# Performance work log

Hardware: AMD Instinct MI355X
Metric: run time of the kernel (lower is better)

Reference implementation:

```python
import jax, jax.numpy as jnp
import numpy as np

B, C_IN, C_OUT, K, H, W, STRIDE, PAD = 64, 64, 128, 3, 32, 32, 1, 1
H_OUT = (H + 2 * PAD - K) // STRIDE + 1
W_OUT = (W + 2 * PAD - K) // STRIDE + 1


def setup_inputs() -> dict:
    key = jax.random.key(0)
    k1, k2 = jax.random.split(key)
    x = jax.random.normal(k1, (B, C_IN, H, W), dtype=jnp.float32)
    fan_in = C_IN * K * K
    weight = jax.random.normal(k2, (C_OUT, H_OUT, W_OUT, C_IN, K, K), dtype=jnp.float32) / np.sqrt(fan_in).astype(np.float32)
    bias = jnp.zeros((C_OUT, H_OUT, W_OUT), dtype=jnp.float32)
    return {"x": x, "weight": weight, "bias": bias}


def _extract_patches(x):
    # x: [B, C, H, W] -> patches [B, C, H_OUT, W_OUT, K, K]
    xp = jnp.pad(x, ((0, 0), (0, 0), (PAD, PAD), (PAD, PAD)))
    rows = []
    for k in range(K):  # small fixed kernel loop (K=3), not a data-dim loop
        cols = []
        for l in range(K):
            cols.append(xp[:, :, k:k + H_OUT * STRIDE:STRIDE, l:l + W_OUT * STRIDE:STRIDE])
        rows.append(jnp.stack(cols, axis=-1))
    return jnp.stack(rows, axis=-2)


def reference(x, weight, bias):
    patches = _extract_patches(x)  # [B, C_IN, H_OUT, W_OUT, K, K]
    # per-location unshared GEMM: out[b,o,h,w] = sum_{i,k,l} weight[o,h,w,i,k,l] * patches[b,i,h,w,k,l]
    out = jnp.einsum('ohwikl,bihwkl->bohw', weight, patches)
    return out + bias[None]
```

## Files before the change

### kernel.cpp

```cpp
#include <hip/hip_runtime.h>


typedef __bf16  bf16x8  __attribute__((ext_vector_type(8)));
typedef float   floatx4 __attribute__((ext_vector_type(4)));

static __device__ inline bf16x8 cvt8(floatx4 a, floatx4 b) {
    bf16x8 r;
    r[0] = (__bf16)a[0]; r[1] = (__bf16)a[1]; r[2] = (__bf16)a[2]; r[3] = (__bf16)a[3];
    r[4] = (__bf16)b[0]; r[5] = (__bf16)b[1]; r[6] = (__bf16)b[2]; r[7] = (__bf16)b[3];
    return r;
}

__global__ __launch_bounds__(256, 3) void prep_kernel(
    const float* __restrict__ x, __bf16* __restrict__ P)
{
    __shared__ float xl[16 * 772];

    const int tid = threadIdx.x;
    const int bid = blockIdx.x;
    const int bq = bid & 3;
    const int ig = (bid >> 2) & 7;
    const int h  = bid >> 5;

    #pragma unroll
    for (int it = 0; it < 12; ++it) {
        int g   = tid + (it << 8);
        int row = g >> 3;
        int sub = g & 7;
        int bl  = row / 24;
        int rem = row - bl * 24;
        int il  = rem / 3;
        int ky  = rem - il * 3;
        int y   = h + ky - 1;
        floatx4 v = {0.f, 0.f, 0.f, 0.f};
        if ((unsigned)y < 32u) {
            const float* src = x + (((size_t)(bq * 16 + bl) * 64 + ig * 8 + il) << 10)
                                 + y * 32 + (sub << 2);
            v = *(const floatx4*)src;
        }
        *(floatx4*)&xl[bl * 772 + il * 96 + ky * 32 + (sub << 2)] = v;
    }
    __syncthreads();

    const int lane = tid & 63;
    const int wv = tid >> 6;
    const int bl = lane & 15;
    const int qq = lane >> 4;

    #pragma unroll 2
    for (int it = 0; it < 18; ++it) {
        int pr  = (it << 4) + (wv << 2) + qq;
        int w   = pr / 9;
        int kol = pr - w * 9;
        int ko  = ig * 9 + kol;
        bf16x8 piece;
        #pragma unroll
        for (int j = 0; j < 8; ++j) {
            int klocal = (kol << 3) + j;
            int il = klocal / 9;
            int p  = klocal - il * 9;
            int ky = p / 3;
            int kx = p - ky * 3;
            int xc = w + kx - 1;
            float v = ((unsigned)xc < 32u) ? xl[bl * 772 + il * 96 + ky * 32 + xc] : 0.0f;
            piece[j] = (__bf16)v;
        }
        int loc   = (h << 5) + w;
        int idx16 = ((ko >> 2) << 8) + (bq << 6) + ((ko & 3) << 4) + bl;
        *(bf16x8*)&P[((size_t)loc * 4608 + idx16) * 8] = piece;
    }
}

__global__ __launch_bounds__(256, 3) void local2d_kernel(
    const __bf16* __restrict__ P,
    const float* __restrict__ weight,
    const float* __restrict__ bias,
    float* __restrict__ out)
{
    __shared__ __bf16 alds[2][12288];

    const int tid  = threadIdx.x;
    const int lane = tid & 63;
    const int wv   = tid >> 6;
    const int ll   = lane & 15;
    const int q    = lane >> 4;

    const int bid = blockIdx.x;
    const int xcd = bid & 7;
    const int w   = (bid >> 3) & 31;
    const int hl  = bid >> 8;
    const int h   = (xcd << 2) + hl;
    const int loc = (h << 5) + w;

    const __bf16* Ploc = P + (size_t)loc * 36864;

    const float* wlane = weight + ((size_t)ll * 1024 + loc) * 576 + (q << 3);
    const float* wptr[8];
    #pragma unroll
    for (int nt = 0; nt < 8; ++nt) wptr[nt] = wlane + (size_t)nt * 9437184;

    floatx4 acc[8];
    #pragma unroll
    for (int nt = 0; nt < 8; ++nt) acc[nt] = (floatx4){0.f, 0.f, 0.f, 0.f};

    #pragma unroll
    for (int it = 0; it < 6; ++it) {
        const __bf16* g = Ploc + ((((it << 2) + wv) << 6) | lane) * 8;
        __builtin_amdgcn_global_load_lds(
            (const __attribute__((address_space(1))) unsigned int*)g,
            (__attribute__((address_space(3))) unsigned int*)&alds[0][(((it << 2) + wv) << 6) * 8],
            16, 0, 0);
    }
    __syncthreads();

    #pragma unroll
    for (int c = 0; c < 3; ++c) {
        if (c < 2) {
            #pragma unroll
            for (int it = 0; it < 6; ++it) {
                const __bf16* g = Ploc + (c + 1) * 12288 + ((((it << 2) + wv) << 6) | lane) * 8;
                __builtin_amdgcn_global_load_lds(
                    (const __attribute__((address_space(1))) unsigned int*)g,
                    (__attribute__((address_space(3))) unsigned int*)&alds[(c + 1) & 1][(((it << 2) + wv) << 6) * 8],
                    16, 0, 0);
            }
        }
        #pragma unroll
        for (int t = 0; t < 6; ++t) {
            bf16x8 af = *(const bf16x8*)&alds[c & 1][((((t << 2) + wv) << 6) | lane) * 8];
            #pragma unroll
            for (int nt = 0; nt < 8; ++nt) {
                const float* src = wptr[nt] + c * 192 + t * 32;
                floatx4 va = *(const floatx4*)src;
                floatx4 vb = *(const floatx4*)(src + 4);
                acc[nt] = __builtin_amdgcn_mfma_f32_16x16x32_bf16(af, cvt8(va, vb), acc[nt], 0, 0, 0);
            }
        }
        if (c < 2) __syncthreads();
    }

    #pragma unroll
    for (int nt = 0; nt < 8; ++nt) {
        int o = (nt << 4) + ll;
        float bv = bias[((size_t)o << 10) + loc];
        #pragma unroll
        for (int r = 0; r < 4; ++r) {
            int m = (wv << 4) + (q << 2) + r;
            out[(((size_t)m << 7) + o) * 1024 + loc] = acc[nt][r] + bv;
        }
    }
}

extern "C" void kernel_launch(void* const* d_in, const int* in_sizes, int n_in,
                              void* d_out, int out_size, void* d_ws, size_t ws_size,
                              hipStream_t stream) {
    const float* x  = (const float*)d_in[0];
    const float* wt = (const float*)d_in[1];
    const float* bi = (const float*)d_in[2];
    float* out = (float*)d_out;
    __bf16* P = (__bf16*)d_ws;
    prep_kernel<<<dim3(1024), dim3(256), 0, stream>>>(x, P);
    local2d_kernel<<<dim3(1024), dim3(256), 0, stream>>>(P, wt, bi, out);
}
```

Measured before the change: 547.2 us.

## Split waves into 2x2 M/N tiles and prefetch weight registers one step ahead

Each wave previously covered 16 batch rows against all 128 output channels, so every wave loaded the full per-location weight slice from global memory. Waves now form a 2x2 grid: each handles 32 batch rows and 64 output channels, reusing each converted weight fragment for two MFMAs and halving redundant global weight reads per block. Weight loads for the next k-step are also issued before the current MFMAs to hide latency. The trade is more accumulator and prefetch registers, which may reduce occupancy under the launch bound of 3.

```diff
diff --git a/kernel.cpp b/kernel.cpp
--- a/kernel.cpp
+++ b/kernel.cpp
@@ -82,6 +82,8 @@
     const int tid  = threadIdx.x;
     const int lane = tid & 63;
     const int wv   = tid >> 6;
+    const int wm   = wv & 1;
+    const int wn   = wv >> 1;
     const int ll   = lane & 15;
     const int q    = lane >> 4;
 
@@ -94,14 +96,18 @@
 
     const __bf16* Ploc = P + (size_t)loc * 36864;
 
-    const float* wlane = weight + ((size_t)ll * 1024 + loc) * 576 + (q << 3);
-    const float* wptr[8];
+    const float* wbase = weight + (size_t)ll * 589824 + (size_t)loc * 576 + (q << 3);
+    const float* wp[4];
     #pragma unroll
-    for (int nt = 0; nt < 8; ++nt) wptr[nt] = wlane + (size_t)nt * 9437184;
+    for (int j = 0; j < 4; ++j)
+        wp[j] = wbase + (size_t)((wn << 2) + j) * 9437184;
 
-    floatx4 acc[8];
+    floatx4 acc0[4], acc1[4];
     #pragma unroll
-    for (int nt = 0; nt < 8; ++nt) acc[nt] = (floatx4){0.f, 0.f, 0.f, 0.f};
+    for (int j = 0; j < 4; ++j) {
+        acc0[j] = (floatx4){0.f, 0.f, 0.f, 0.f};
+        acc1[j] = (floatx4){0.f, 0.f, 0.f, 0.f};
+    }
 
     #pragma unroll
     for (int it = 0; it < 6; ++it) {
@@ -125,28 +131,53 @@
                     16, 0, 0);
             }
         }
+
+        floatx4 cva[4], cvb[4], nva[4], nvb[4];
+        #pragma unroll
+        for (int j = 0; j < 4; ++j) {
+            const float* s = wp[j] + c * 192;
+            cva[j] = *(const floatx4*)s;
+            cvb[j] = *(const floatx4*)(s + 4);
+        }
+
         #pragma unroll
         for (int t = 0; t < 6; ++t) {
-            bf16x8 af = *(const bf16x8*)&alds[c & 1][((((t << 2) + wv) << 6) | lane) * 8];
+            bf16x8 af0 = *(const bf16x8*)&alds[c & 1][((((t << 2) + (wm << 1)) << 6) | lane) * 8];
+            bf16x8 af1 = *(const bf16x8*)&alds[c & 1][((((t << 2) + (wm << 1) + 1) << 6) | lane) * 8];
+            if (t < 5) {
+                #pragma unroll
+                for (int j = 0; j < 4; ++j) {
+                    const float* s = wp[j] + c * 192 + (t + 1) * 32;
+                    nva[j] = *(const floatx4*)s;
+                    nvb[j] = *(const floatx4*)(s + 4);
+                }
+            }
             #pragma unroll
-            for (int nt = 0; nt < 8; ++nt) {
-                const float* src = wptr[nt] + c * 192 + t * 32;
-                floatx4 va = *(const floatx4*)src;
-                floatx4 vb = *(const floatx4*)(src + 4);
-                acc[nt] = __builtin_amdgcn_mfma_f32_16x16x32_bf16(af, cvt8(va, vb), acc[nt], 0, 0, 0);
+            for (int j = 0; j < 4; ++j) {
+                bf16x8 bw = cvt8(cva[j], cvb[j]);
+                acc0[j] = __builtin_amdgcn_mfma_f32_16x16x32_bf16(af0, bw, acc0[j], 0, 0, 0);
+                acc1[j] = __builtin_amdgcn_mfma_f32_16x16x32_bf16(af1, bw, acc1[j], 0, 0, 0);
+            }
+            if (t < 5) {
+                #pragma unroll
+                for (int j = 0; j < 4; ++j) { cva[j] = nva[j]; cvb[j] = nvb[j]; }
             }
         }
         if (c < 2) __syncthreads();
     }
 
     #pragma unroll
-    for (int nt = 0; nt < 8; ++nt) {
-        int o = (nt << 4) + ll;
-        float bv = bias[((size_t)o << 10) + loc];
+    for (int fi = 0; fi < 2; ++fi) {
         #pragma unroll
-        for (int r = 0; r < 4; ++r) {
-            int m = (wv << 4) + (q << 2) + r;
-            out[(((size_t)m << 7) + o) * 1024 + loc] = acc[nt][r] + bv;
+        for (int j = 0; j < 4; ++j) {
+            int o = (((wn << 2) + j) << 4) + ll;
+            float bv = bias[((size_t)o << 10) + loc];
+            #pragma unroll
+            for (int r = 0; r < 4; ++r) {
+                int m = (((wm << 1) + fi) << 4) + (q << 2) + r;
+                float v = (fi == 0 ? acc0[j][r] : acc1[j][r]) + bv;
+                out[(((size_t)m << 7) + o) * 1024 + loc] = v;
+            }
         }
     }
 }
```

Result: faster. 516.1 us (-5.7%).
